# Kernel tuning notes

Hardware: AMD Instinct MI355X
Metric: run time of the kernel (lower is better)

Reference implementation:

```python
import jax, jax.numpy as jnp
import numpy as np


def _conv(x, w, b, stride, pad):
    # NCHW conv, OIHW weights, bias add
    y = jax.lax.conv_general_dilated(
        x, w, (stride, stride), [(pad, pad), (pad, pad)],
        dimension_numbers=('NCHW', 'OIHW', 'NCHW'))
    return y + b[None, :, None, None]


def setup_inputs() -> dict:
    key = jax.random.key(0)
    ks = jax.random.split(key, 8)
    s = 0.05  # small init so SiLU chains stay numerically tame
    f32 = jnp.float32
    return {
        'x': jax.random.normal(ks[0], (8, 3, 640, 640), f32),
        'w0': jax.random.normal(ks[1], (32, 3, 3, 3), f32) * s,
        'b0': jnp.zeros((32,), f32),
        'w1': jax.random.normal(ks[2], (64, 32, 3, 3), f32) * s,
        'b1': jnp.zeros((64,), f32),
        'wc0': jax.random.normal(ks[3], (64, 64, 1, 1), f32) * s,
        'bc0': jnp.zeros((64,), f32),
        'wb1': jax.random.normal(ks[4], (32, 32, 3, 3), f32) * s,
        'bb1': jnp.zeros((32,), f32),
        'wb2': jax.random.normal(ks[5], (32, 32, 3, 3), f32) * s,
        'bb2': jnp.zeros((32,), f32),
        'wc1': jax.random.normal(ks[6], (64, 96, 1, 1), f32) * s,
        'bc1': jnp.zeros((64,), f32),
        'w3': jax.random.normal(ks[7], (128, 64, 3, 3), f32) * s,
        'b3': jnp.zeros((128,), f32),
    }


def reference(x, w0, b0, w1, b1, wc0, bc0, wb1, bb1, wb2, bb2, wc1, bc1, w3, b3):
    silu = jax.nn.silu
    # stem: conv0 (s2) + conv1 (s2), each Conv+SiLU
    h = silu(_conv(x, w0, b0, 2, 1))     # [B,32,320,320]
    h = silu(_conv(h, w1, b1, 2, 1))     # [B,64,160,160]
    # C2f block: 1x1 conv, split channels in half, residual bottleneck, concat, 1x1 conv
    y = silu(_conv(h, wc0, bc0, 1, 0))   # [B,64,160,160]
    x1, x2 = jnp.split(y, 2, axis=1)     # each [B,32,160,160]
    b = silu(_conv(x2, wb1, bb1, 1, 1))
    b = silu(_conv(b, wb2, bb2, 1, 1))
    b = x2 + b                           # shortcut=True bottleneck
    cat = jnp.concatenate([x1, x2, b], axis=1)  # [B,96,160,160] == 192*w
    h = silu(_conv(cat, wc1, bc1, 1, 0))  # [B,64,160,160]
    # conv3: downsample stage (s2)
    out = silu(_conv(h, w3, b3, 2, 1))    # [B,128,80,80]
    return out
```

## Files before the change

kernel.cpp:

```cpp
#include <hip/hip_runtime.h>
#include <hip/hip_bf16.h>

typedef __attribute__((ext_vector_type(8))) short short8;
typedef __attribute__((ext_vector_type(16))) float f32x16;
typedef __attribute__((ext_vector_type(4))) float f32x4;
typedef __attribute__((ext_vector_type(4))) unsigned int uint4v;
typedef __attribute__((ext_vector_type(4))) unsigned short ushort4v;

__device__ __forceinline__ float silu_f(float v) {
    return v * __builtin_amdgcn_rcpf(1.0f + __expf(-v));
}
__device__ __forceinline__ unsigned short bfhi(float v) {
    __hip_bfloat16 h = __float2bfloat16(v);
    return *reinterpret_cast<unsigned short*>(&h);
}
__device__ __forceinline__ float bf2f(unsigned short u) {
    __hip_bfloat16 h;
    *reinterpret_cast<unsigned short*>(&h) = u;
    return __bfloat162float(h);
}

__global__ __launch_bounds__(256) void prep_small(
    const float* __restrict__ w1, const float* __restrict__ wc0,
    const float* __restrict__ wb1, const float* __restrict__ wb2,
    const float* __restrict__ wc1, const float* __restrict__ w0,
    unsigned short* __restrict__ arena)
{
    const int u = blockIdx.x * 256 + threadIdx.x;
    if (u >= 6016) return;
    const int lane = u & 63, pf = u >> 6;
    float wv[8];
    if (pf < 36) {
        const int q = pf, cc = q & 1, rnd = (q >> 1) & 1, tap = q >> 2;
        const int co = cc * 32 + (lane & 31), ci0 = rnd * 16 + (lane >> 5) * 8;
        #pragma unroll
        for (int j = 0; j < 8; ++j) wv[j] = w1[(co * 32 + ci0 + j) * 9 + tap];
    } else if (pf < 44) {
        const int q = pf - 36, cc = q & 1, rnd = q >> 1;
        const int co = cc * 32 + (lane & 31), ci0 = rnd * 16 + (lane >> 5) * 8;
        #pragma unroll
        for (int j = 0; j < 8; ++j) wv[j] = wc0[co * 64 + ci0 + j];
    } else if (pf < 62) {
        const int q = pf - 44, rnd = q & 1, tap = q >> 1;
        const int co = lane & 31, ci0 = rnd * 16 + (lane >> 5) * 8;
        #pragma unroll
        for (int j = 0; j < 8; ++j) wv[j] = wb1[(co * 32 + ci0 + j) * 9 + tap];
    } else if (pf < 80) {
        const int q = pf - 62, rnd = q & 1, tap = q >> 1;
        const int co = lane & 31, ci0 = rnd * 16 + (lane >> 5) * 8;
        #pragma unroll
        for (int j = 0; j < 8; ++j) wv[j] = wb2[(co * 32 + ci0 + j) * 9 + tap];
    } else if (pf < 92) {
        const int q = pf - 80, cc = q & 1, rnd = q >> 1;
        const int co = cc * 32 + (lane & 31), ci0 = rnd * 16 + (lane >> 5) * 8;
        #pragma unroll
        for (int j = 0; j < 8; ++j) wv[j] = wc1[co * 96 + ci0 + j];
    } else {
        const int co = lane & 31;
        const int k0 = (pf - 92) * 16 + (lane >> 5) * 8;
        #pragma unroll
        for (int j = 0; j < 8; ++j) {
            const int k = k0 + j;
            wv[j] = (k < 27) ? w0[(co * 3 + k / 9) * 9 + (k % 9)] : 0.0f;
        }
    }
    unsigned short hs[8], ls[8];
    #pragma unroll
    for (int j = 0; j < 8; ++j) {
        unsigned short hh = bfhi(wv[j]);
        hs[j] = hh; ls[j] = bfhi(wv[j] - bf2f(hh));
    }
    *reinterpret_cast<short8*>(&arena[pf * 1024 + lane * 8])       = *(short8*)hs;
    *reinterpret_cast<short8*>(&arena[pf * 1024 + 512 + lane * 8]) = *(short8*)ls;
}

__global__ __launch_bounds__(256) void prep_w3(
    const float* __restrict__ w3, unsigned short* __restrict__ arena)
{
    const int u = blockIdx.x * 256 + threadIdx.x;
    const int lane = u & 63, pf = u >> 6;
    const int cc = pf & 1, rr = (pf >> 1) & 3, t9 = pf >> 3;
    const int tap = t9 % 9, cg = t9 / 9;
    const int co = cg * 64 + cc * 32 + (lane & 31);
    const int ci0 = rr * 16 + (lane >> 5) * 8;
    unsigned short hs[8], ls[8];
    #pragma unroll
    for (int j = 0; j < 8; ++j) {
        float wv = w3[(co * 64 + ci0 + j) * 9 + tap];
        unsigned short hh = bfhi(wv);
        hs[j] = hh; ls[j] = bfhi(wv - bf2f(hh));
    }
    *reinterpret_cast<short8*>(&arena[pf * 1024 + lane * 8])       = *(short8*)hs;
    *reinterpret_cast<short8*>(&arena[pf * 1024 + 512 + lane * 8]) = *(short8*)ls;
}

struct GDesc {
    int rc, Bsafe, Y, X;
    bool validR, valid, fastw;
};

__device__ __forceinline__ GDesc stem_desc(int g, int p, int ox0, int oy0) {
    GDesc d;
    d.rc = g * 32 + p;
    d.validR = d.rc < 325;
    const int rec_c = d.validR ? d.rc : 324;
    int gp, row, col;
    if (rec_c < 64)       { gp = 0; row = rec_c >> 5; col = rec_c & 31; }
    else if (rec_c < 130) { gp = 1; int r2 = rec_c - 64;  row = r2 / 33; col = r2 - row * 33; }
    else if (rec_c < 226) { gp = 2; int r2 = rec_c - 130; row = r2 >> 5; col = r2 & 31; }
    else                  { gp = 3; int r2 = rec_c - 226; row = r2 / 33; col = r2 - row * 33; }
    const int gr = (gp >= 2) ? oy0 - 1 + row : oy0 + row;
    const int gc = (gp & 1)  ? ox0 - 1 + col : ox0 + col;
    d.valid = d.validR && ((unsigned)gr < 160u) && ((unsigned)gc < 160u);
    d.Y = 2 * gr + (gp >> 1);
    d.X = 2 * gc + (gp & 1);
    d.Bsafe = d.valid ? (1280 * d.Y + 2 * d.X) : 641;
    const bool interior = d.valid && gr > 0 && gr < 159 && gc > 0 && gc < 159;
    d.fastw = __all(interior);
    return d;
}

__device__ __forceinline__ void stem_issue(
    int Bsafe, const int* doff, const float* __restrict__ xb, float* xv)
{
    #pragma unroll
    for (int idx = 0; idx < 16; ++idx) {
        int a = Bsafe + doff[idx];
        a = max(a, 0);
        a = min(a, 1228799);
        xv[idx] = xb[a];
    }
}

__device__ __forceinline__ void stem_process(
    const GDesc& d, const float* xv, unsigned short* lds,
    const unsigned short* __restrict__ wfr, const float* __restrict__ b0,
    int h, int h8, int lane)
{
    f32x16 a0;
    #pragma unroll
    for (int q = 0; q < 4; ++q) {
        f32x4 b4 = *reinterpret_cast<const f32x4*>(&b0[q * 8 + 4 * h]);
        #pragma unroll
        for (int r2 = 0; r2 < 4; ++r2) a0[q * 4 + r2] = b4[r2];
    }

    #pragma unroll
    for (int rnd = 0; rnd < 2; ++rnd) {
        unsigned short hs[8], ls[8];
        if (d.fastw) {
            #pragma unroll
            for (int j = 0; j < 8; ++j) {
                float v = xv[rnd * 8 + j];
                if (rnd == 1 && j >= 3) v = (h == 0) ? v : 0.0f;
                unsigned short hh = bfhi(v);
                hs[j] = hh; ls[j] = bfhi(v - bf2f(hh));
            }
        } else {
            #pragma unroll
            for (int j = 0; j < 8; ++j) {
                const int k = rnd * 16 + h8 + j;
                const int ci = (k * 57) >> 9;
                const int tap = k - 9 * ci;
                const int dy = (tap * 11) >> 5, dx = tap - 3 * dy;
                const int iy = 2 * d.Y + dy - 1;
                const int ix = 2 * d.X + dx - 1;
                bool ok = d.valid && ((unsigned)iy < 640u) && ((unsigned)ix < 640u);
                if (rnd == 1 && j >= 3) ok = ok && (h == 0);
                float v = ok ? xv[rnd * 8 + j] : 0.0f;
                unsigned short hh = bfhi(v);
                hs[j] = hh; ls[j] = bfhi(v - bf2f(hh));
            }
        }
        short8 Bh = *(short8*)hs, Bl = *(short8*)ls;
        const unsigned short* fb = wfr + (92 + rnd) * 1024 + lane * 8;
        short8 Awh = *reinterpret_cast<const short8*>(fb);
        short8 Awl = *reinterpret_cast<const short8*>(fb + 512);
        a0 = __builtin_amdgcn_mfma_f32_32x32x16_bf16(Awh, Bh, a0, 0, 0, 0);
        a0 = __builtin_amdgcn_mfma_f32_32x32x16_bf16(Awh, Bl, a0, 0, 0, 0);
        a0 = __builtin_amdgcn_mfma_f32_32x32x16_bf16(Awl, Bh, a0, 0, 0, 0);
    }

    if (d.validR) {
        const int pm = d.rc & 7;
        #pragma unroll
        for (int q = 0; q < 4; ++q) {
            ushort4v hv, lv;
            #pragma unroll
            for (int r2 = 0; r2 < 4; ++r2) {
                float v = d.valid ? silu_f(a0[q * 4 + r2]) : 0.0f;
                unsigned short hh = bfhi(v);
                hv[r2] = hh; lv[r2] = bfhi(v - bf2f(hh));
            }
            *reinterpret_cast<ushort4v*>(&lds[d.rc * 64 + (((2 * q)     ^ pm) * 8) + 4 * h]) = hv;
            *reinterpret_cast<ushort4v*>(&lds[d.rc * 64 + (((2 * q + 1) ^ pm) * 8) + 4 * h]) = lv;
        }
    }
}

__global__ __launch_bounds__(256, 4) void stem_fused(
    const float* __restrict__ x, const unsigned short* __restrict__ wfr,
    const unsigned short* __restrict__ wc0fr, const float* __restrict__ b0,
    const float* __restrict__ bias, const float* __restrict__ bc0,
    unsigned short* __restrict__ ycl)
{
    __shared__ unsigned short lds[20800];
    const int tid = threadIdx.x;
    const int wv = tid >> 6, lane = tid & 63;
    const int p = lane & 31, h = lane >> 5;
    const int r = wv >> 1, cc = wv & 1;
    const int bx = blockIdx.x % 5, by = blockIdx.x / 5;
    const int ox0 = bx * 32, oy0 = by * 2;
    const int n = blockIdx.z;
    const float* xb = x + (long)n * 1228800;

    const int h8 = h * 8;
    int doff[16];
    #pragma unroll
    for (int idx = 0; idx < 16; ++idx) {
        const int k = (idx >> 3) * 16 + h8 + (idx & 7);
        if (k < 27) {
            const int ci = (k * 57) >> 9;
            const int tap = k - 9 * ci;
            const int dy = (tap * 11) >> 5, dx = tap - 3 * dy;
            doff[idx] = ci * 409600 + (dy - 1) * 640 + (dx - 1);
        } else {
            doff[idx] = 0;
        }
    }

    {
        GDesc d0 = stem_desc(wv, p, ox0, oy0);
        float xva[16];
        stem_issue(d0.Bsafe, doff, xb, xva);

        GDesc d1 = stem_desc(wv + 4, p, ox0, oy0);
        float xvb[16];
        stem_issue(d1.Bsafe, doff, xb, xvb);

        stem_process(d0, xva, lds, wfr, b0, h, h8, lane);

        if (wv < 3) {
            GDesc d2 = stem_desc(wv + 8, p, ox0, oy0);
            stem_issue(d2.Bsafe, doff, xb, xva);
            stem_process(d1, xvb, lds, wfr, b0, h, h8, lane);
            stem_process(d2, xva, lds, wfr, b0, h, h8, lane);
        } else {
            stem_process(d1, xvb, lds, wfr, b0, h, h8, lane);
        }
    }
    __syncthreads();

    f32x16 acc;
    #pragma unroll
    for (int q = 0; q < 4; ++q) {
        f32x4 b4 = *reinterpret_cast<const f32x4*>(&bias[cc * 32 + q * 8 + 4 * h]);
        #pragma unroll
        for (int r2 = 0; r2 < 4; ++r2) acc[q * 4 + r2] = b4[r2];
    }
    #pragma unroll
    for (int c = 0; c < 2; ++c) {
        #pragma unroll
        for (int tap = 0; tap < 9; ++tap) {
            const int dy = tap / 3 - 1, dx = tap % 3 - 1;
            const int ppy = dy & 1, ppx = dx & 1;
            const int toy = ppy ? ((dy == -1) ? 0 : 1) : 0;
            const int tox = ppx ? ((dx == -1) ? 0 : 1) : 0;
            const int gp = ppy * 2 + ppx;
            const int base = (gp == 0) ? 0 : (gp == 1) ? 64 : (gp == 2) ? 130 : 226;
            const int W = ppx ? 33 : 32;
            const int rec = base + (ppy ? (r + toy) : r) * W + (p + tox);
            const unsigned short* t = &lds[rec * 64];
            const int pm = rec & 7;
            short8 Bh = *reinterpret_cast<const short8*>(t + (((4 * c + 2 * h)     ^ pm) * 8));
            short8 Bl = *reinterpret_cast<const short8*>(t + (((4 * c + 2 * h + 1) ^ pm) * 8));
            const unsigned short* fb = wfr + ((tap * 2 + c) * 2 + cc) * 1024 + lane * 8;
            short8 Awh = *reinterpret_cast<const short8*>(fb);
            short8 Awl = *reinterpret_cast<const short8*>(fb + 512);
            acc = __builtin_amdgcn_mfma_f32_32x32x16_bf16(Awh, Bh, acc, 0, 0, 0);
            acc = __builtin_amdgcn_mfma_f32_32x32x16_bf16(Awh, Bl, acc, 0, 0, 0);
            acc = __builtin_amdgcn_mfma_f32_32x32x16_bf16(Awl, Bh, acc, 0, 0, 0);
        }
    }

    __syncthreads();
    {
        const int rec2 = r * 32 + p;
        #pragma unroll
        for (int q = 0; q < 4; ++q) {
            ushort4v hv, lv;
            #pragma unroll
            for (int r2 = 0; r2 < 4; ++r2) {
                float v = silu_f(acc[q * 4 + r2]);
                unsigned short hh = bfhi(v);
                hv[r2] = hh; lv[r2] = bfhi(v - bf2f(hh));
            }
            const int lsh = (2 * (cc * 4 + q))     ^ (rec2 & 15);
            const int lsl = (2 * (cc * 4 + q) + 1) ^ (rec2 & 15);
            *reinterpret_cast<ushort4v*>(&lds[rec2 * 128 + lsh * 8 + 4 * h]) = hv;
            *reinterpret_cast<ushort4v*>(&lds[rec2 * 128 + lsl * 8 + 4 * h]) = lv;
        }
    }
    __syncthreads();

    f32x16 a2;
    #pragma unroll
    for (int q = 0; q < 4; ++q) {
        f32x4 b4 = *reinterpret_cast<const f32x4*>(&bc0[cc * 32 + q * 8 + 4 * h]);
        #pragma unroll
        for (int r2 = 0; r2 < 4; ++r2) a2[q * 4 + r2] = b4[r2];
    }
    {
        const int rec2 = r * 32 + p;
        #pragma unroll
        for (int rnd = 0; rnd < 4; ++rnd) {
            const int sh = (4 * rnd + 2 * h)     ^ (rec2 & 15);
            const int sl = (4 * rnd + 2 * h + 1) ^ (rec2 & 15);
            short8 Bh = *reinterpret_cast<const short8*>(&lds[rec2 * 128 + sh * 8]);
            short8 Bl = *reinterpret_cast<const short8*>(&lds[rec2 * 128 + sl * 8]);
            const unsigned short* fb = wc0fr + (rnd * 2 + cc) * 1024 + lane * 8;
            short8 Awh = *reinterpret_cast<const short8*>(fb);
            short8 Awl = *reinterpret_cast<const short8*>(fb + 512);
            a2 = __builtin_amdgcn_mfma_f32_32x32x16_bf16(Awh, Bh, a2, 0, 0, 0);
            a2 = __builtin_amdgcn_mfma_f32_32x32x16_bf16(Awh, Bl, a2, 0, 0, 0);
            a2 = __builtin_amdgcn_mfma_f32_32x32x16_bf16(Awl, Bh, a2, 0, 0, 0);
        }
    }

    const int oy = oy0 + r;
    unsigned short* op = ycl + ((long)n * 25600 + (long)oy * 160 + ox0 + p) * 128;
    #pragma unroll
    for (int q = 0; q < 4; ++q) {
        ushort4v hv, lv;
        #pragma unroll
        for (int r2 = 0; r2 < 4; ++r2) {
            float v = silu_f(a2[q * 4 + r2]);
            unsigned short hh = bfhi(v);
            hv[r2] = hh; lv[r2] = bfhi(v - bf2f(hh));
        }
        const int gq = cc * 4 + q;
        *reinterpret_cast<ushort4v*>(op + gq * 16 + 4 * h)     = hv;
        *reinterpret_cast<ushort4v*>(op + gq * 16 + 8 + 4 * h) = lv;
    }
}

template <bool RESID>
__global__ __launch_bounds__(512, 4) void wb3x3(
    const unsigned short* __restrict__ in, int inRec, int inSlot0,
    const unsigned short* __restrict__ wfr, const float* __restrict__ bias,
    unsigned short* __restrict__ outb, const unsigned short* __restrict__ resid)
{
    __shared__ unsigned short lds[21760];
    const int tid = threadIdx.x;
    const int wv = tid >> 6, lane = tid & 63;
    const int p = lane & 31, h = lane >> 5;
    const int bx = blockIdx.x % 5, by = blockIdx.x / 5;
    const int ox0 = bx * 32, oy0 = by * 8;
    const int n = blockIdx.z;

    for (int u = tid; u < 2720; u += 512) {
        const int rec = u >> 3, s = u & 7;
        const int row = rec / 34, col = rec - row * 34;
        const int gr = oy0 - 1 + row, gc = ox0 - 1 + col;
        uint4v val = {0, 0, 0, 0};
        if (gr >= 0 && gr < 160 && gc >= 0 && gc < 160)
            val = *reinterpret_cast<const uint4v*>(
                in + ((long)n * 25600 + gr * 160 + gc) * inRec + (inSlot0 + s) * 8);
        *reinterpret_cast<uint4v*>(&lds[rec * 64 + ((s ^ (rec & 7)) * 8)]) = val;
    }

    f32x16 acc;
    #pragma unroll
    for (int q = 0; q < 4; ++q) {
        f32x4 b4 = *reinterpret_cast<const f32x4*>(&bias[q * 8 + 4 * h]);
        #pragma unroll
        for (int r = 0; r < 4; ++r) acc[q * 4 + r] = b4[r];
    }
    __syncthreads();

    #pragma unroll
    for (int tap = 0; tap < 9; ++tap) {
        const int dy = tap / 3 - 1, dx = tap % 3 - 1;
        const int rec = (wv + dy + 1) * 34 + (p + dx + 1);
        const unsigned short* t = &lds[rec * 64];
        short8 Bh[2], Bl[2];
        #pragma unroll
        for (int rnd = 0; rnd < 2; ++rnd) {
            Bh[rnd] = *reinterpret_cast<const short8*>(t + (((rnd*4 + 2*h)     ^ (rec & 7)) * 8));
            Bl[rnd] = *reinterpret_cast<const short8*>(t + (((rnd*4 + 2*h + 1) ^ (rec & 7)) * 8));
        }
        #pragma unroll
        for (int rnd = 0; rnd < 2; ++rnd) {
            const unsigned short* fb = wfr + (tap * 2 + rnd) * 1024 + lane * 8;
            short8 Awh = *reinterpret_cast<const short8*>(fb);
            short8 Awl = *reinterpret_cast<const short8*>(fb + 512);
            acc = __builtin_amdgcn_mfma_f32_32x32x16_bf16(Awh, Bh[rnd], acc, 0, 0, 0);
            acc = __builtin_amdgcn_mfma_f32_32x32x16_bf16(Awh, Bl[rnd], acc, 0, 0, 0);
            acc = __builtin_amdgcn_mfma_f32_32x32x16_bf16(Awl, Bh[rnd], acc, 0, 0, 0);
        }
    }

    const int oy = oy0 + wv;
    const long prow = (long)n * 25600 + (long)oy * 160 + ox0 + p;
    unsigned short* op = outb + prow * 64;
    const unsigned short* rp = RESID ? resid + prow * 128 : nullptr;
    #pragma unroll
    for (int q = 0; q < 4; ++q) {
        ushort4v hv, lv;
        float vs[4];
        #pragma unroll
        for (int r = 0; r < 4; ++r) vs[r] = silu_f(acc[q * 4 + r]);
        if (RESID) {
            ushort4v rh = *reinterpret_cast<const ushort4v*>(rp + (q + 4) * 16 + 4 * h);
            ushort4v rl = *reinterpret_cast<const ushort4v*>(rp + (q + 4) * 16 + 8 + 4 * h);
            #pragma unroll
            for (int r = 0; r < 4; ++r) vs[r] += bf2f(rh[r]) + bf2f(rl[r]);
        }
        #pragma unroll
        for (int r = 0; r < 4; ++r) {
            unsigned short hh = bfhi(vs[r]);
            hv[r] = hh; lv[r] = bfhi(vs[r] - bf2f(hh));
        }
        *reinterpret_cast<ushort4v*>(op + q * 16 + 4 * h)     = hv;
        *reinterpret_cast<ushort4v*>(op + q * 16 + 8 + 4 * h) = lv;
    }
}

template <int R1, int R2, bool POUT>
__global__ __launch_bounds__(512, 4) void wc1x1(
    const unsigned short* __restrict__ in1, int rec1,
    const unsigned short* __restrict__ in2, int rec2,
    const unsigned short* __restrict__ wfr, const float* __restrict__ bias,
    unsigned short* __restrict__ outb)
{
    constexpr int RT = R1 + R2;
    const int tid = threadIdx.x;
    const int wv = tid >> 6, lane = tid & 63;
    const int p = lane & 31, h = lane >> 5;
    const int n = blockIdx.z;
    const int px0 = blockIdx.x * 512;

    f32x16 acc[2][2];
    #pragma unroll
    for (int cc = 0; cc < 2; ++cc)
        #pragma unroll
        for (int q = 0; q < 4; ++q) {
            f32x4 b4 = *reinterpret_cast<const f32x4*>(&bias[cc * 32 + q * 8 + 4 * h]);
            #pragma unroll
            for (int r = 0; r < 4; ++r) { acc[cc][0][q*4+r] = b4[r]; acc[cc][1][q*4+r] = b4[r]; }
        }

    #pragma unroll
    for (int rnd = 0; rnd < RT; ++rnd) {
        const unsigned short* bp = (rnd < R1) ? in1 : in2;
        const int recN = (rnd < R1) ? rec1 : rec2;
        const int s0 = 4 * ((rnd < R1) ? rnd : rnd - R1);
        #pragma unroll
        for (int k = 0; k < 2; ++k) {
            const int px = px0 + (wv * 2 + k) * 32 + p;
            const unsigned short* sp = bp + ((long)n * 25600 + px) * recN + (s0 + 2 * h) * 8;
            short8 Bh = *reinterpret_cast<const short8*>(sp);
            short8 Bl = *reinterpret_cast<const short8*>(sp + 8);
            #pragma unroll
            for (int cc = 0; cc < 2; ++cc) {
                const unsigned short* fb = wfr + (rnd * 2 + cc) * 1024 + lane * 8;
                short8 Awh = *reinterpret_cast<const short8*>(fb);
                short8 Awl = *reinterpret_cast<const short8*>(fb + 512);
                acc[cc][k] = __builtin_amdgcn_mfma_f32_32x32x16_bf16(Awh, Bh, acc[cc][k], 0, 0, 0);
                acc[cc][k] = __builtin_amdgcn_mfma_f32_32x32x16_bf16(Awh, Bl, acc[cc][k], 0, 0, 0);
                acc[cc][k] = __builtin_amdgcn_mfma_f32_32x32x16_bf16(Awl, Bh, acc[cc][k], 0, 0, 0);
            }
        }
    }

    #pragma unroll
    for (int k = 0; k < 2; ++k) {
        const int px = px0 + (wv * 2 + k) * 32 + p;
        unsigned short* op;
        if (POUT) {
            const int y = px / 160, xx = px % 160;
            const int pl = (y & 1) * 2 + (xx & 1);
            op = outb + (((long)n * 4 + pl) * 6400 + (y >> 1) * 80 + (xx >> 1)) * 128;
        } else {
            op = outb + ((long)n * 25600 + px) * 128;
        }
        #pragma unroll
        for (int cc = 0; cc < 2; ++cc)
            #pragma unroll
            for (int q = 0; q < 4; ++q) {
                ushort4v hv, lv;
                #pragma unroll
                for (int r = 0; r < 4; ++r) {
                    float v = silu_f(acc[cc][k][q * 4 + r]);
                    unsigned short hh = bfhi(v);
                    hv[r] = hh; lv[r] = bfhi(v - bf2f(hh));
                }
                const int gq = cc * 4 + q;
                *reinterpret_cast<ushort4v*>(op + gq * 16 + 4 * h)     = hv;
                *reinterpret_cast<ushort4v*>(op + gq * 16 + 8 + 4 * h) = lv;
            }
    }
}

__global__ __launch_bounds__(512, 4) void conv3_one(
    const unsigned short* __restrict__ h2p, const unsigned short* __restrict__ wfr,
    const float* __restrict__ bias, float* __restrict__ outf)
{
    __shared__ unsigned short lds[34848];
    const int tid = threadIdx.x;
    const int wv = tid >> 6, lane = tid & 63;
    const int p = lane & 31, h = lane >> 5;
    const int bx = blockIdx.x % 5, by = blockIdx.x / 5;
    const int ox0 = bx * 16, oy0 = by * 16;
    const int cg = blockIdx.y;
    const int co0 = cg * 64;
    const int n = blockIdx.z;

    f32x16 acc[2];
    #pragma unroll
    for (int cc = 0; cc < 2; ++cc)
        #pragma unroll
        for (int q = 0; q < 4; ++q) {
            f32x4 b4 = *reinterpret_cast<const f32x4*>(&bias[co0 + cc * 32 + q * 8 + 4 * h]);
            #pragma unroll
            for (int r = 0; r < 4; ++r) acc[cc][q * 4 + r] = b4[r];
        }

    for (int rr = 0; rr < 4; ++rr) {
        __syncthreads();
        for (int u = tid; u < 4356; u += 512) {
            const int rec = u >> 2, s = u & 3;
            int gp, row, col;
            if (rec < 256)      { gp = 0; row = rec >> 4; col = rec & 15; }
            else if (rec < 528) { gp = 1; int r2 = rec - 256; row = r2 / 17; col = r2 - row * 17; }
            else if (rec < 800) { gp = 2; int r2 = rec - 528; row = r2 >> 4; col = r2 & 15; }
            else                { gp = 3; int r2 = rec - 800; row = r2 / 17; col = r2 - row * 17; }
            const int gr = (gp >= 2) ? oy0 - 1 + row : oy0 + row;
            const int gc = (gp & 1)  ? ox0 - 1 + col : ox0 + col;
            uint4v val = {0, 0, 0, 0};
            if (gr >= 0 && gr < 80 && gc >= 0 && gc < 80)
                val = *reinterpret_cast<const uint4v*>(
                    h2p + (((long)n * 4 + gp) * 6400 + gr * 80 + gc) * 128 + (rr * 4 + s) * 8);
            *reinterpret_cast<uint4v*>(&lds[rec * 32 + ((s ^ ((rec >> 1) & 3)) * 8)]) = val;
        }
        __syncthreads();

        #pragma unroll
        for (int tap = 0; tap < 9; ++tap) {
            const int dy = tap / 3 - 1, dx = tap % 3 - 1;
            const int ppy = dy & 1, ppx = dx & 1;
            const int toy = ppy ? ((dy == -1) ? 0 : 1) : 0;
            const int tox = ppx ? ((dx == -1) ? 0 : 1) : 0;
            const int gp = ppy * 2 + ppx;
            const int base = (gp == 0) ? 0 : (gp == 1) ? 256 : (gp == 2) ? 528 : 800;
            const int W = ppx ? 17 : 16;
            const int rl = wv * 2 + (p >> 4), cl = p & 15;
            const int rec = base + (ppy ? (rl + toy) : rl) * W + (cl + tox);
            const unsigned short* t = &lds[rec * 32];
            const int pm = (rec >> 1) & 3;
            short8 Bh = *reinterpret_cast<const short8*>(t + (((2*h)     ^ pm) * 8));
            short8 Bl = *reinterpret_cast<const short8*>(t + (((2*h + 1) ^ pm) * 8));
            #pragma unroll
            for (int cc = 0; cc < 2; ++cc) {
                const unsigned short* fb =
                    wfr + (((cg * 9 + tap) * 4 + rr) * 2 + cc) * 1024 + lane * 8;
                short8 Awh = *reinterpret_cast<const short8*>(fb);
                short8 Awl = *reinterpret_cast<const short8*>(fb + 512);
                acc[cc] = __builtin_amdgcn_mfma_f32_32x32x16_bf16(Awh, Bh, acc[cc], 0, 0, 0);
                acc[cc] = __builtin_amdgcn_mfma_f32_32x32x16_bf16(Awh, Bl, acc[cc], 0, 0, 0);
                acc[cc] = __builtin_amdgcn_mfma_f32_32x32x16_bf16(Awl, Bh, acc[cc], 0, 0, 0);
            }
        }
    }

    const int rl = wv * 2 + (p >> 4);
    const int oy = oy0 + rl;
    const int pxg = oy * 80 + ox0 + (p & 15);
    #pragma unroll
    for (int cc = 0; cc < 2; ++cc)
        #pragma unroll
        for (int q = 0; q < 4; ++q)
            #pragma unroll
            for (int r = 0; r < 4; ++r) {
                const int co = co0 + cc * 32 + q * 8 + 4 * h + r;
                outf[((long)n * 128 + co) * 6400 + pxg] = silu_f(acc[cc][q * 4 + r]);
            }
}

extern "C" void kernel_launch(void* const* d_in, const int* in_sizes, int n_in,
                              void* d_out, int out_size, void* d_ws, size_t ws_size,
                              hipStream_t stream) {
    const float* x   = (const float*)d_in[0];
    const float* w0  = (const float*)d_in[1];
    const float* b0  = (const float*)d_in[2];
    const float* w1  = (const float*)d_in[3];
    const float* b1  = (const float*)d_in[4];
    const float* wc0 = (const float*)d_in[5];
    const float* bc0 = (const float*)d_in[6];
    const float* wb1 = (const float*)d_in[7];
    const float* bb1 = (const float*)d_in[8];
    const float* wb2 = (const float*)d_in[9];
    const float* bb2 = (const float*)d_in[10];
    const float* wc1 = (const float*)d_in[11];
    const float* bc1 = (const float*)d_in[12];
    const float* w3  = (const float*)d_in[13];
    const float* b3  = (const float*)d_in[14];

    unsigned short* u = (unsigned short*)d_ws;
    unsigned short* ycl  = u + 52428800L;
    unsigned short* b1cl = u + 26214400L;
    unsigned short* bcl  = u + 39321600L;
    unsigned short* h2p  = u;
    unsigned short* w3a  = u + 26214400L;

    unsigned short* wsa = (unsigned short*)d_out;
    unsigned short* a_conv1 = wsa;
    unsigned short* a_wc0   = wsa + 36 * 1024;
    unsigned short* a_wb1   = wsa + 44 * 1024;
    unsigned short* a_wb2   = wsa + 62 * 1024;
    unsigned short* a_wc1   = wsa + 80 * 1024;

    prep_small<<<dim3(24, 1, 1), dim3(256, 1, 1), 0, stream>>>(
        w1, wc0, wb1, wb2, wc1, w0, wsa);

    stem_fused<<<dim3(400, 1, 8), dim3(256, 1, 1), 0, stream>>>(
        x, a_conv1, a_wc0, b0, b1, bc0, ycl);

    wb3x3<false><<<dim3(100, 1, 8), dim3(512, 1, 1), 0, stream>>>(
        ycl, 128, 8, a_wb1, bb1, b1cl, nullptr);

    wb3x3<true><<<dim3(100, 1, 8), dim3(512, 1, 1), 0, stream>>>(
        b1cl, 64, 0, a_wb2, bb2, bcl, ycl);

    prep_w3<<<dim3(36, 1, 1), dim3(256, 1, 1), 0, stream>>>(w3, w3a);

    wc1x1<4, 2, true><<<dim3(50, 1, 8), dim3(512, 1, 1), 0, stream>>>(
        ycl, 128, bcl, 64, a_wc1, bc1, h2p);

    conv3_one<<<dim3(25, 2, 8), dim3(512, 1, 1), 0, stream>>>(h2p, w3a, b3, (float*)d_out);
}
```

Measured before the change: 237.5 us.

## Fuse second bottleneck 3x3 conv with residual and C2f 1x1 concat conv

```diff
diff --git a/kernel.cpp b/kernel.cpp
--- a/kernel.cpp
+++ b/kernel.cpp
@@ -344,11 +344,10 @@
     }
 }
 
-template <bool RESID>
 __global__ __launch_bounds__(512, 4) void wb3x3(
     const unsigned short* __restrict__ in, int inRec, int inSlot0,
     const unsigned short* __restrict__ wfr, const float* __restrict__ bias,
-    unsigned short* __restrict__ outb, const unsigned short* __restrict__ resid)
+    unsigned short* __restrict__ outb)
 {
     __shared__ unsigned short lds[21760];
     const int tid = threadIdx.x;
@@ -403,102 +402,165 @@
     const int oy = oy0 + wv;
     const long prow = (long)n * 25600 + (long)oy * 160 + ox0 + p;
     unsigned short* op = outb + prow * 64;
-    const unsigned short* rp = RESID ? resid + prow * 128 : nullptr;
     #pragma unroll
     for (int q = 0; q < 4; ++q) {
         ushort4v hv, lv;
-        float vs[4];
-        #pragma unroll
-        for (int r = 0; r < 4; ++r) vs[r] = silu_f(acc[q * 4 + r]);
-        if (RESID) {
-            ushort4v rh = *reinterpret_cast<const ushort4v*>(rp + (q + 4) * 16 + 4 * h);
-            ushort4v rl = *reinterpret_cast<const ushort4v*>(rp + (q + 4) * 16 + 8 + 4 * h);
-            #pragma unroll
-            for (int r = 0; r < 4; ++r) vs[r] += bf2f(rh[r]) + bf2f(rl[r]);
-        }
         #pragma unroll
         for (int r = 0; r < 4; ++r) {
-            unsigned short hh = bfhi(vs[r]);
-            hv[r] = hh; lv[r] = bfhi(vs[r] - bf2f(hh));
+            float v = silu_f(acc[q * 4 + r]);
+            unsigned short hh = bfhi(v);
+            hv[r] = hh; lv[r] = bfhi(v - bf2f(hh));
         }
         *reinterpret_cast<ushort4v*>(op + q * 16 + 4 * h)     = hv;
         *reinterpret_cast<ushort4v*>(op + q * 16 + 8 + 4 * h) = lv;
     }
 }
 
-template <int R1, int R2, bool POUT>
-__global__ __launch_bounds__(512, 4) void wc1x1(
-    const unsigned short* __restrict__ in1, int rec1,
-    const unsigned short* __restrict__ in2, int rec2,
-    const unsigned short* __restrict__ wfr, const float* __restrict__ bias,
-    unsigned short* __restrict__ outb)
-{
-    constexpr int RT = R1 + R2;
+__global__ __launch_bounds__(512, 4) void wb2_wc1(
+    const unsigned short* __restrict__ b1cl, const unsigned short* __restrict__ ycl,
+    const unsigned short* __restrict__ wfr2, const unsigned short* __restrict__ wfrc,
+    const float* __restrict__ bb2, const float* __restrict__ bc1,
+    unsigned short* __restrict__ h2p)
+{
+    __shared__ unsigned short lds[21760];
     const int tid = threadIdx.x;
     const int wv = tid >> 6, lane = tid & 63;
     const int p = lane & 31, h = lane >> 5;
+    const int bx = blockIdx.x % 5, by = blockIdx.x / 5;
+    const int ox0 = bx * 32, oy0 = by * 8;
     const int n = blockIdx.z;
-    const int px0 = blockIdx.x * 512;
-
-    f32x16 acc[2][2];
-    #pragma unroll
-    for (int cc = 0; cc < 2; ++cc)
+
+    for (int u = tid; u < 2720; u += 512) {
+        const int rec = u >> 3, s = u & 7;
+        const int row = rec / 34, col = rec - row * 34;
+        const int gr = oy0 - 1 + row, gc = ox0 - 1 + col;
+        uint4v val = {0, 0, 0, 0};
+        if (gr >= 0 && gr < 160 && gc >= 0 && gc < 160)
+            val = *reinterpret_cast<const uint4v*>(
+                b1cl + ((long)n * 25600 + gr * 160 + gc) * 64 + s * 8);
+        *reinterpret_cast<uint4v*>(&lds[rec * 64 + ((s ^ (rec & 7)) * 8)]) = val;
+    }
+
+    f32x16 acc;
+    #pragma unroll
+    for (int q = 0; q < 4; ++q) {
+        f32x4 b4 = *reinterpret_cast<const f32x4*>(&bb2[q * 8 + 4 * h]);
+        #pragma unroll
+        for (int r = 0; r < 4; ++r) acc[q * 4 + r] = b4[r];
+    }
+    __syncthreads();
+
+    #pragma unroll
+    for (int tap = 0; tap < 9; ++tap) {
+        const int dy = tap / 3 - 1, dx = tap % 3 - 1;
+        const int rec = (wv + dy + 1) * 34 + (p + dx + 1);
+        const unsigned short* t = &lds[rec * 64];
+        short8 Bh[2], Bl[2];
+        #pragma unroll
+        for (int rnd = 0; rnd < 2; ++rnd) {
+            Bh[rnd] = *reinterpret_cast<const short8*>(t + (((rnd*4 + 2*h)     ^ (rec & 7)) * 8));
+            Bl[rnd] = *reinterpret_cast<const short8*>(t + (((rnd*4 + 2*h + 1) ^ (rec & 7)) * 8));
+        }
+        #pragma unroll
+        for (int rnd = 0; rnd < 2; ++rnd) {
+            const unsigned short* fb = wfr2 + (tap * 2 + rnd) * 1024 + lane * 8;
+            short8 Awh = *reinterpret_cast<const short8*>(fb);
+            short8 Awl = *reinterpret_cast<const short8*>(fb + 512);
+            acc = __builtin_amdgcn_mfma_f32_32x32x16_bf16(Awh, Bh[rnd], acc, 0, 0, 0);
+            acc = __builtin_amdgcn_mfma_f32_32x32x16_bf16(Awh, Bl[rnd], acc, 0, 0, 0);
+            acc = __builtin_amdgcn_mfma_f32_32x32x16_bf16(Awl, Bh[rnd], acc, 0, 0, 0);
+        }
+    }
+
+    const int oy = oy0 + wv;
+    const long prow = (long)n * 25600 + (long)oy * 160 + ox0 + p;
+    const unsigned short* rp = ycl + prow * 128;
+    float vs[16];
+    #pragma unroll
+    for (int q = 0; q < 4; ++q) {
+        ushort4v rh = *reinterpret_cast<const ushort4v*>(rp + (q + 4) * 16 + 4 * h);
+        ushort4v rl = *reinterpret_cast<const ushort4v*>(rp + (q + 4) * 16 + 8 + 4 * h);
+        #pragma unroll
+        for (int r = 0; r < 4; ++r)
+            vs[q * 4 + r] = silu_f(acc[q * 4 + r]) + bf2f(rh[r]) + bf2f(rl[r]);
+    }
+
+    __syncthreads();
+    {
+        const int rec = wv * 32 + p;
+        const int pm = rec & 7;
         #pragma unroll
         for (int q = 0; q < 4; ++q) {
-            f32x4 b4 = *reinterpret_cast<const f32x4*>(&bias[cc * 32 + q * 8 + 4 * h]);
-            #pragma unroll
-            for (int r = 0; r < 4; ++r) { acc[cc][0][q*4+r] = b4[r]; acc[cc][1][q*4+r] = b4[r]; }
-        }
-
-    #pragma unroll
-    for (int rnd = 0; rnd < RT; ++rnd) {
-        const unsigned short* bp = (rnd < R1) ? in1 : in2;
-        const int recN = (rnd < R1) ? rec1 : rec2;
-        const int s0 = 4 * ((rnd < R1) ? rnd : rnd - R1);
-        #pragma unroll
-        for (int k = 0; k < 2; ++k) {
-            const int px = px0 + (wv * 2 + k) * 32 + p;
-            const unsigned short* sp = bp + ((long)n * 25600 + px) * recN + (s0 + 2 * h) * 8;
+            ushort4v hv, lv;
+            #pragma unroll
+            for (int r = 0; r < 4; ++r) {
+                unsigned short hh = bfhi(vs[q * 4 + r]);
+                hv[r] = hh; lv[r] = bfhi(vs[q * 4 + r] - bf2f(hh));
+            }
+            *reinterpret_cast<ushort4v*>(&lds[rec * 64 + (((2 * q)     ^ pm) * 8) + 4 * h]) = hv;
+            *reinterpret_cast<ushort4v*>(&lds[rec * 64 + (((2 * q + 1) ^ pm) * 8) + 4 * h]) = lv;
+        }
+    }
+    __syncthreads();
+
+    const int cc = wv & 1;
+    #pragma unroll
+    for (int g2 = 0; g2 < 2; ++g2) {
+        const int rowg = (wv >> 1) + g2 * 4;
+        const int oyg = oy0 + rowg;
+        const long pg = (long)n * 25600 + (long)oyg * 160 + ox0 + p;
+
+        f32x16 a2;
+        #pragma unroll
+        for (int q = 0; q < 4; ++q) {
+            f32x4 b4 = *reinterpret_cast<const f32x4*>(&bc1[cc * 32 + q * 8 + 4 * h]);
+            #pragma unroll
+            for (int r = 0; r < 4; ++r) a2[q * 4 + r] = b4[r];
+        }
+
+        #pragma unroll
+        for (int rnd = 0; rnd < 4; ++rnd) {
+            const unsigned short* sp = ycl + pg * 128 + (rnd * 4 + 2 * h) * 8;
             short8 Bh = *reinterpret_cast<const short8*>(sp);
             short8 Bl = *reinterpret_cast<const short8*>(sp + 8);
-            #pragma unroll
-            for (int cc = 0; cc < 2; ++cc) {
-                const unsigned short* fb = wfr + (rnd * 2 + cc) * 1024 + lane * 8;
-                short8 Awh = *reinterpret_cast<const short8*>(fb);
-                short8 Awl = *reinterpret_cast<const short8*>(fb + 512);
-                acc[cc][k] = __builtin_amdgcn_mfma_f32_32x32x16_bf16(Awh, Bh, acc[cc][k], 0, 0, 0);
-                acc[cc][k] = __builtin_amdgcn_mfma_f32_32x32x16_bf16(Awh, Bl, acc[cc][k], 0, 0, 0);
-                acc[cc][k] = __builtin_amdgcn_mfma_f32_32x32x16_bf16(Awl, Bh, acc[cc][k], 0, 0, 0);
-            }
-        }
-    }
-
-    #pragma unroll
-    for (int k = 0; k < 2; ++k) {
-        const int px = px0 + (wv * 2 + k) * 32 + p;
-        unsigned short* op;
-        if (POUT) {
-            const int y = px / 160, xx = px % 160;
-            const int pl = (y & 1) * 2 + (xx & 1);
-            op = outb + (((long)n * 4 + pl) * 6400 + (y >> 1) * 80 + (xx >> 1)) * 128;
-        } else {
-            op = outb + ((long)n * 25600 + px) * 128;
-        }
-        #pragma unroll
-        for (int cc = 0; cc < 2; ++cc)
-            #pragma unroll
-            for (int q = 0; q < 4; ++q) {
-                ushort4v hv, lv;
-                #pragma unroll
-                for (int r = 0; r < 4; ++r) {
-                    float v = silu_f(acc[cc][k][q * 4 + r]);
-                    unsigned short hh = bfhi(v);
-                    hv[r] = hh; lv[r] = bfhi(v - bf2f(hh));
-                }
-                const int gq = cc * 4 + q;
-                *reinterpret_cast<ushort4v*>(op + gq * 16 + 4 * h)     = hv;
-                *reinterpret_cast<ushort4v*>(op + gq * 16 + 8 + 4 * h) = lv;
-            }
+            const unsigned short* fb = wfrc + (rnd * 2 + cc) * 1024 + lane * 8;
+            short8 Awh = *reinterpret_cast<const short8*>(fb);
+            short8 Awl = *reinterpret_cast<const short8*>(fb + 512);
+            a2 = __builtin_amdgcn_mfma_f32_32x32x16_bf16(Awh, Bh, a2, 0, 0, 0);
+            a2 = __builtin_amdgcn_mfma_f32_32x32x16_bf16(Awh, Bl, a2, 0, 0, 0);
+            a2 = __builtin_amdgcn_mfma_f32_32x32x16_bf16(Awl, Bh, a2, 0, 0, 0);
+        }
+        const int recb = rowg * 32 + p;
+        const int pmb = recb & 7;
+        #pragma unroll
+        for (int rnd = 0; rnd < 2; ++rnd) {
+            const unsigned short* t = &lds[recb * 64];
+            short8 Bh = *reinterpret_cast<const short8*>(t + (((4*rnd + 2*h)     ^ pmb) * 8));
+            short8 Bl = *reinterpret_cast<const short8*>(t + (((4*rnd + 2*h + 1) ^ pmb) * 8));
+            const unsigned short* fb = wfrc + ((4 + rnd) * 2 + cc) * 1024 + lane * 8;
+            short8 Awh = *reinterpret_cast<const short8*>(fb);
+            short8 Awl = *reinterpret_cast<const short8*>(fb + 512);
+            a2 = __builtin_amdgcn_mfma_f32_32x32x16_bf16(Awh, Bh, a2, 0, 0, 0);
+            a2 = __builtin_amdgcn_mfma_f32_32x32x16_bf16(Awh, Bl, a2, 0, 0, 0);
+            a2 = __builtin_amdgcn_mfma_f32_32x32x16_bf16(Awl, Bh, a2, 0, 0, 0);
+        }
+
+        const int xx = ox0 + p;
+        const int pl = (oyg & 1) * 2 + (xx & 1);
+        unsigned short* op = h2p + (((long)n * 4 + pl) * 6400 + (oyg >> 1) * 80 + (xx >> 1)) * 128;
+        #pragma unroll
+        for (int q = 0; q < 4; ++q) {
+            ushort4v hv, lv;
+            #pragma unroll
+            for (int r = 0; r < 4; ++r) {
+                float v = silu_f(a2[q * 4 + r]);
+                unsigned short hh = bfhi(v);
+                hv[r] = hh; lv[r] = bfhi(v - bf2f(hh));
+            }
+            const int gq = cc * 4 + q;
+            *reinterpret_cast<ushort4v*>(op + gq * 16 + 4 * h)     = hv;
+            *reinterpret_cast<ushort4v*>(op + gq * 16 + 8 + 4 * h) = lv;
+        }
     }
 }
 
@@ -609,7 +671,6 @@
     unsigned short* u = (unsigned short*)d_ws;
     unsigned short* ycl  = u + 52428800L;
     unsigned short* b1cl = u + 26214400L;
-    unsigned short* bcl  = u + 39321600L;
     unsigned short* h2p  = u;
     unsigned short* w3a  = u + 26214400L;
 
@@ -626,16 +687,13 @@
     stem_fused<<<dim3(400, 1, 8), dim3(256, 1, 1), 0, stream>>>(
         x, a_conv1, a_wc0, b0, b1, bc0, ycl);
 
-    wb3x3<false><<<dim3(100, 1, 8), dim3(512, 1, 1), 0, stream>>>(
-        ycl, 128, 8, a_wb1, bb1, b1cl, nullptr);
-
-    wb3x3<true><<<dim3(100, 1, 8), dim3(512, 1, 1), 0, stream>>>(
-        b1cl, 64, 0, a_wb2, bb2, bcl, ycl);
+    wb3x3<<<dim3(100, 1, 8), dim3(512, 1, 1), 0, stream>>>(
+        ycl, 128, 8, a_wb1, bb1, b1cl);
+
+    wb2_wc1<<<dim3(100, 1, 8), dim3(512, 1, 1), 0, stream>>>(
+        b1cl, ycl, a_wb2, a_wc1, bb2, bc1, h2p);
 
     prep_w3<<<dim3(36, 1, 1), dim3(256, 1, 1), 0, stream>>>(w3, w3a);
 
-    wc1x1<4, 2, true><<<dim3(50, 1, 8), dim3(512, 1, 1), 0, stream>>>(
-        ycl, 128, bcl, 64, a_wc1, bc1, h2p);
-
     conv3_one<<<dim3(25, 2, 8), dim3(512, 1, 1), 0, stream>>>(h2p, w3a, b3, (float*)d_out);
 }
```

New measurement: 233.0 us (median of 2 runs). No clear change (-1.9%).
